# Kernel optimization log

Hardware: AMD Instinct MI355X
Metric: run time of the kernel (lower is better)

The kernel has to match this reference:

```python
import jax, jax.numpy as jnp
import numpy as np

B, N, E, D, H, L = 1024, 64, 1024, 128, 4, 2
C = D // H          # per-head out_channels
K = 5               # options per attribute
LN_EPS = 1e-5


def setup_inputs() -> dict:
    key = jax.random.key(0)
    ks = jax.random.split(key, 22)
    s = 0.05
    inp = {
        'x': jax.random.randint(ks[0], (B, N), 0, K),
        'edge_index': jax.random.randint(ks[1], (2, E), 0, N),
        'edge_attr': jax.random.uniform(ks[2], (E, 1), jnp.float32),
        # tokenizer params
        'attr_emb': jax.random.normal(ks[3], (N, D), jnp.float32) * s,
        'opt_emb': jax.random.normal(ks[4], (N, K, D), jnp.float32) * s,
        'prior': jnp.ones((N, 1), jnp.float32),
        # GATv2 params, stacked over layers
        'Wl': jax.random.normal(ks[5], (L, D, D), jnp.float32) * s,
        'bl': jnp.zeros((L, D), jnp.float32),
        'Wr': jax.random.normal(ks[6], (L, D, D), jnp.float32) * s,
        'br': jnp.zeros((L, D), jnp.float32),
        'We': jax.random.normal(ks[7], (L, 1, D), jnp.float32) * s,
        'att': jax.random.normal(ks[8], (L, H, C), jnp.float32) * s,
        'conv_bias': jnp.zeros((L, D), jnp.float32),
        'ln_g': jnp.ones((L, D), jnp.float32),
        'ln_b': jnp.zeros((L, D), jnp.float32),
        # reliability head
        'W1': jax.random.normal(ks[9], (2 * D, D), jnp.float32) * s,
        'b1': jnp.zeros((D,), jnp.float32),
        'W2': jax.random.normal(ks[10], (D, 1), jnp.float32) * s,
        'b2': jnp.zeros((1,), jnp.float32),
    }
    return inp


def _forward(x, edge_index, edge_attr, attr_emb, opt_emb, prior,
             Wl, bl, Wr, br, We, att, conv_bias, ln_g, ln_b, W1, b1, W2, b2):
    Bb, n = x.shape
    # Tokenizer: token_i = p_i * (E_attr[i] + E_val[i](x_i))
    val = opt_emb[jnp.arange(n)[None, :], x]                 # [B,n,D]
    T0 = (attr_emb[None] + val) * prior[None]                # [B,n,D]

    src, dst = edge_index[0], edge_index[1]
    h = T0
    for l in range(Wl.shape[0]):
        xl = (h @ Wl[l] + bl[l]).reshape(Bb, n, H, C)        # source transform
        xr = (h @ Wr[l] + br[l]).reshape(Bb, n, H, C)        # target transform
        e = (edge_attr @ We[l]).reshape(1, E, H, C)          # edge embedding
        msg = xl[:, src]                                     # [B,E,H,C]
        z = jax.nn.leaky_relu(msg + xr[:, dst] + e, 0.2)
        alpha = jnp.einsum('behc,hc->beh', z, att[l])        # [B,E,H]
        # segment softmax over incoming edges per target node
        mx = jnp.full((Bb, n, H), -jnp.inf, alpha.dtype).at[:, dst].max(alpha)
        ex = jnp.exp(alpha - mx[:, dst])
        den = jnp.zeros((Bb, n, H), alpha.dtype).at[:, dst].add(ex)
        a = ex / den[:, dst]                                 # normalized attention
        out = jnp.zeros((Bb, n, H, C), h.dtype).at[:, dst].add(msg * a[..., None])
        g = out.reshape(Bb, n, D) + conv_bias[l]
        mu = g.mean(-1, keepdims=True)
        var = g.var(-1, keepdims=True)
        g = (g - mu) / jnp.sqrt(var + LN_EPS) * ln_g[l] + ln_b[l]
        g = jax.nn.elu(g)
        h = h + g                                            # residual

    hat_T = jnp.concatenate([T0, h], axis=-1)                # [B,n,2D]
    rel = jax.nn.sigmoid(jax.nn.relu(hat_T @ W1 + b1) @ W2 + b2)[..., 0]  # [B,n]
    rw = rel[..., None]
    f_scale = (h * rw).sum(1) / (rw.sum(1) + 1e-8)           # [B,D]
    return f_scale, rel, hat_T


def reference(x, edge_index, edge_attr, attr_emb, opt_emb, prior,
              Wl, bl, Wr, br, We, att, conv_bias, ln_g, ln_b, W1, b1, W2, b2):
    return _forward(x, edge_index, edge_attr, attr_emb, opt_emb, prior,
                    Wl, bl, Wr, br, We, att, conv_bias, ln_g, ln_b, W1, b1, W2, b2)
```

## Files before the change

### kernel.cpp

```cpp
#include <hip/hip_runtime.h>
#include <hip/hip_bf16.h>

#define Bv 1024
#define Nv 64
#define Ev 1024
#define Dv 128
#define Hv 4
#define Lv 2
#define Kv 5
#define PAD 130

typedef __hip_bfloat16 bf16;
typedef __attribute__((ext_vector_type(8))) short bf16x8_t;
typedef __attribute__((ext_vector_type(4))) float f32x4_t;
typedef __attribute__((ext_vector_type(2))) float f32x2_t;

__device__ __forceinline__ float b2f(bf16 v) { return __bfloat162float(v); }
__device__ __forceinline__ bf16  f2b(float v) { return __float2bfloat16(v); }

__device__ bf16 g_pWl[(size_t)Lv * 2 * Dv * Dv];
__device__ bf16 g_pWr[(size_t)Lv * 2 * Dv * Dv];
__device__ bf16 g_pW1[(size_t)2 * 2 * Dv * Dv];
__device__ float g_K[Lv * Hv];
__device__ unsigned short g_spk[Ev];
__device__ float          g_sea[Ev];
__device__ int            g_off[Nv + 1];

__device__ __forceinline__ f32x2_t unpack2v(unsigned int u) {
    union { unsigned int u; float f; } a, b;
    a.u = u << 16;
    b.u = u & 0xffff0000u;
    return (f32x2_t){a.f, b.f};
}

__device__ __forceinline__ unsigned int pack2v(f32x2_t v) {
    union { bf16 b; unsigned short u; } lo, hi;
    lo.b = f2b(v.x); hi.b = f2b(v.y);
    return (unsigned int)lo.u | ((unsigned int)hi.u << 16);
}

__device__ __forceinline__ bf16x8_t load_a_frag(const bf16* buf, int elem_idx) {
    const unsigned int* p = (const unsigned int*)buf;
    union { bf16x8_t v; unsigned int u[4]; } r;
    int d = elem_idx >> 1;
    r.u[0] = p[d]; r.u[1] = p[d + 1]; r.u[2] = p[d + 2]; r.u[3] = p[d + 3];
    return r.v;
}

__device__ void pack_mat(const float* __restrict__ W, bf16* __restrict__ out,
                         int K, int tid, int nth)
{
    const int total = K * 128;
    for (int e = tid; e < total; e += nth) {
        int f    = e >> 9;
        int rem  = e & 511;
        int lane = rem >> 3;
        int i    = rem & 7;
        int kk   = f >> 3;
        int nt   = f & 7;
        int col  = nt * 16 + (lane & 15);
        int k    = kk * 32 + (lane >> 4) * 8 + i;
        float w  = W[k * 128 + col];
        bf16 hi  = f2b(w);
        out[e]         = hi;
        out[total + e] = f2b(w - b2f(hi));
    }
}

__global__ void prep(const int* __restrict__ edge_index, const float* __restrict__ edge_attr,
                     const float* __restrict__ Wl, const float* __restrict__ Wr,
                     const float* __restrict__ W1, const float* __restrict__ We,
                     const float* __restrict__ att)
{
    const int bid = blockIdx.x;
    if (bid == 0) {
        __shared__ int cnt[Nv];
        int tid = threadIdx.x;
        if (tid < Nv) cnt[tid] = 0;
        __syncthreads();
        for (int e = tid; e < Ev; e += blockDim.x)
            atomicAdd(&cnt[edge_index[Ev + e]], 1);
        __syncthreads();
        if (tid == 0) {
            int s = 0;
            for (int t = 0; t < Nv; ++t) { int c = cnt[t]; g_off[t] = s; cnt[t] = s; s += c; }
            g_off[Nv] = s;
        }
        __syncthreads();
        for (int e = tid; e < Ev; e += blockDim.x) {
            int s = edge_index[e];
            int d = edge_index[Ev + e];
            int pos = atomicAdd(&cnt[d], 1);
            g_spk[pos] = (unsigned short)(s | (d << 6));
            g_sea[pos] = edge_attr[e];
        }
        return;
    }
    const int nth = (gridDim.x - 1) * 256;
    const int tid = (bid - 1) * 256 + threadIdx.x;
    for (int l = 0; l < Lv; ++l) {
        pack_mat(Wl + (size_t)l * Dv * Dv, g_pWl + (size_t)l * 2 * Dv * Dv, Dv, tid, nth);
        pack_mat(Wr + (size_t)l * Dv * Dv, g_pWr + (size_t)l * 2 * Dv * Dv, Dv, tid, nth);
    }
    pack_mat(W1, g_pW1, 2 * Dv, tid, nth);
    if (bid == 1 && threadIdx.x < Lv * Hv) {
        int l = threadIdx.x / Hv, h = threadIdx.x % Hv;
        float k = 0.f;
        for (int c = 0; c < 32; ++c)
            k += att[l * Dv + h * 32 + c] * We[l * Dv + h * 32 + c];
        g_K[threadIdx.x] = 0.2f * k;
    }
}

__global__ __launch_bounds__(512, 2)
void gat_fused(const int* __restrict__ x,
               const float* __restrict__ attr_emb,
               const float* __restrict__ opt_emb, const float* __restrict__ prior,
               const float* __restrict__ bl, const float* __restrict__ br,
               const float* __restrict__ conv_bias, const float* __restrict__ ln_g,
               const float* __restrict__ ln_b,
               const float* __restrict__ b1, const float* __restrict__ W2,
               const float* __restrict__ b2,
               const float* __restrict__ We, const float* __restrict__ att,
               float* __restrict__ out_fscale, float* __restrict__ out_rel,
               float* __restrict__ out_hatT)
{
    const int b = blockIdx.x;
    const int tid = threadIdx.x;

    __shared__ __align__(16) bf16 hs [Nv * PAD];
    __shared__ __align__(16) bf16 xls[Nv * PAD];
    __shared__ __align__(16) bf16 xrs[Nv * PAD];
    __shared__ bf16 alphas[Ev * Hv];
    __shared__ __align__(16) float red [Nv * 8];
    __shared__ __align__(16) float red2[Nv * 8];
    __shared__ __align__(16) float wecol[Dv];
    __shared__ __align__(16) float attv [Dv];
    __shared__ float relbuf[Nv];
    __shared__ __align__(16) unsigned short spk[Ev];
    __shared__ __align__(16) float sea[Ev];
    __shared__ int off[Nv + 1];

    for (int i = tid; i < Ev; i += 512) {
        spk[i] = g_spk[i];
        sea[i] = g_sea[i];
    }
    if (tid < Nv + 1) off[tid] = g_off[tid];
    for (int idx = tid; idx < Nv * Dv; idx += 512) {
        int n = idx >> 7, d = idx & 127;
        float t0 = (attr_emb[n * Dv + d] + opt_emb[(n * Kv + x[b * Nv + n]) * Dv + d])
                   * prior[n];
        hs[n * PAD + d] = f2b(t0);
    }

    for (int l = 0; l < Lv; ++l) {
        if (tid < Dv) {
            wecol[tid] = We[l * Dv + tid];
            attv[tid]  = att[l * Dv + tid];
        }
        __syncthreads();

        {
            const int w = tid >> 6, lane = tid & 63;
            const int row16 = lane & 15, kg = lane >> 4;
            const bf16* pB = (w < 4) ? (g_pWl + (size_t)l * 2 * Dv * Dv)
                                     : (g_pWr + (size_t)l * 2 * Dv * Dv);
            const int wc = (w & 3) * 32;
            bf16* dst = (w < 4) ? xls : xrs;
            const float* bias = (w < 4) ? (bl + l * Dv) : (br + l * Dv);

            #pragma unroll
            for (int nt = 0; nt < 2; ++nt) {
                f32x4_t acc[4];
                #pragma unroll
                for (int mt = 0; mt < 4; ++mt)
                    acc[mt] = (f32x4_t){0.f, 0.f, 0.f, 0.f};

                #pragma unroll
                for (int kk = 0; kk < 4; ++kk) {
                    const int kb = kk * 32 + kg * 8;
                    const int f = kk * 8 + (w & 3) * 2 + nt;
                    bf16x8_t bh  = *(const bf16x8_t*)&pB[(size_t)(f * 64 + lane) * 8];
                    bf16x8_t blo = *(const bf16x8_t*)&pB[Dv * Dv + (size_t)(f * 64 + lane) * 8];
                    #pragma unroll
                    for (int mt = 0; mt < 4; ++mt) {
                        bf16x8_t a = load_a_frag(hs, (mt * 16 + row16) * PAD + kb);
                        acc[mt] = __builtin_amdgcn_mfma_f32_16x16x32_bf16(a, bh,  acc[mt], 0, 0, 0);
                        acc[mt] = __builtin_amdgcn_mfma_f32_16x16x32_bf16(a, blo, acc[mt], 0, 0, 0);
                    }
                }
                const int col = wc + nt * 16 + row16;
                const float bv = bias[col];
                #pragma unroll
                for (int mt = 0; mt < 4; ++mt) {
                    #pragma unroll
                    for (int r = 0; r < 4; ++r) {
                        const int row = mt * 16 + kg * 4 + r;
                        dst[row * PAD + col] = f2b(acc[mt][r] + bv);
                    }
                }
            }
        }
        __syncthreads();

        {
            const int t = tid & 63, h = (tid >> 6) & 3, half = tid >> 8;
            const int ch0 = h * 32 + half * 16;
            f32x2_t dl2 = {0.f, 0.f}, dr2 = {0.f, 0.f};
            #pragma unroll
            for (int c = 0; c < 16; c += 2) {
                f32x2_t a2 = *(const f32x2_t*)&attv[ch0 + c];
                dl2 += a2 * unpack2v(*(const unsigned int*)&xls[t * PAD + ch0 + c]);
                dr2 += a2 * unpack2v(*(const unsigned int*)&xrs[t * PAD + ch0 + c]);
            }
            red [t * 8 + h * 2 + half] = dl2.x + dl2.y;
            red2[t * 8 + h * 2 + half] = dr2.x + dr2.y;
        }
        __syncthreads();

        {
            const int h = (tid >> 6) & 3, half = tid >> 8, lane = tid & 63;
            const float k02 = g_K[l * Hv + h];
            const f32x2_t zero2 = {0.f, 0.f};
            for (int it = 0; it < 8; ++it) {
                int pos = (half * 8 + it) * 64 + lane;
                int pk = spk[pos];
                int s = pk & 63, t = (pk >> 6) & 63;
                float ea = sea[pos];
                f32x2_t ea2 = {ea, ea};
                f32x2_t acc2 = {0.f, 0.f};
                int bs = s * PAD + h * 32, bt = t * PAD + h * 32;
                #pragma unroll
                for (int c = 0; c < 32; c += 2) {
                    f32x2_t xl2 = unpack2v(*(const unsigned int*)&xls[bs + c]);
                    f32x2_t xr2 = unpack2v(*(const unsigned int*)&xrs[bt + c]);
                    f32x2_t we2 = *(const f32x2_t*)&wecol[h * 32 + c];
                    f32x2_t at2 = *(const f32x2_t*)&attv [h * 32 + c];
                    f32x2_t v   = xl2 + xr2 + ea2 * we2;
                    acc2 += at2 * __builtin_elementwise_max(v, zero2);
                }
                float dL = red [s * 8 + h * 2] + red [s * 8 + h * 2 + 1];
                float dR = red2[t * 8 + h * 2] + red2[t * 8 + h * 2 + 1];
                float alpha = 0.2f * (dL + dR) + k02 * ea + 0.8f * (acc2.x + acc2.y);
                alphas[pos * Hv + h] = f2b(alpha);
            }
        }
        __syncthreads();

        {
            const int t = tid & 63, h = (tid >> 6) & 3, half = tid >> 8;
            const int ch0 = h * 32 + half * 16;
            int beg = off[t], end = off[t + 1];
            float mx = -3e38f;
            for (int idx = beg; idx < end; ++idx)
                mx = fmaxf(mx, b2f(alphas[idx * Hv + h]));
            f32x2_t acc2[8];
            #pragma unroll
            for (int j = 0; j < 8; ++j) acc2[j] = (f32x2_t){0.f, 0.f};
            float den = 0.f;
            for (int idx = beg; idx < end; ++idx) {
                int s = spk[idx] & 63;
                float ex = expf(b2f(alphas[idx * Hv + h]) - mx);
                den += ex;
                f32x2_t ex2 = {ex, ex};
                int bs = s * PAD + ch0;
                #pragma unroll
                for (int j = 0; j < 8; ++j)
                    acc2[j] += ex2 * unpack2v(*(const unsigned int*)&xls[bs + 2 * j]);
            }
            float inv_den = (end > beg) ? 1.f / den : 0.f;
            f32x2_t id2 = {inv_den, inv_den};
            f32x2_t sum2 = {0.f, 0.f}, sq2 = {0.f, 0.f};
            #pragma unroll
            for (int j = 0; j < 8; ++j) {
                f32x2_t cb = *(const f32x2_t*)&conv_bias[l * Dv + ch0 + 2 * j];
                f32x2_t g  = acc2[j] * id2 + cb;
                acc2[j] = g;
                sum2 += g; sq2 += g * g;
            }
            red [t * 8 + h * 2 + half] = sum2.x + sum2.y;
            red2[t * 8 + h * 2 + half] = sq2.x + sq2.y;
            __syncthreads();
            float mu = 0.f, ms = 0.f;
            #pragma unroll
            for (int j = 0; j < 8; ++j) { mu += red[t * 8 + j]; ms += red2[t * 8 + j]; }
            mu *= (1.f / 128.f); ms *= (1.f / 128.f);
            float rstd = rsqrtf(ms - mu * mu + 1e-5f);
            f32x2_t mu2 = {mu, mu}, rs2 = {rstd, rstd};
            #pragma unroll
            for (int j = 0; j < 8; ++j) {
                f32x2_t lg = *(const f32x2_t*)&ln_g[l * Dv + ch0 + 2 * j];
                f32x2_t lb = *(const f32x2_t*)&ln_b[l * Dv + ch0 + 2 * j];
                f32x2_t g  = (acc2[j] - mu2) * rs2 * lg + lb;
                g.x = g.x > 0.f ? g.x : (expf(g.x) - 1.f);
                g.y = g.y > 0.f ? g.y : (expf(g.y) - 1.f);
                unsigned int* hp = (unsigned int*)&hs[t * PAD + ch0 + 2 * j];
                f32x2_t hv = unpack2v(*hp) + g;
                *hp = pack2v(hv);
            }
        }
        __syncthreads();
    }

    if (tid < Dv) wecol[tid] = W2[tid];
    for (int idx = tid; idx < Nv * Dv; idx += 512) {
        int n = idx >> 7, d = idx & 127;
        float t0 = (attr_emb[n * Dv + d] + opt_emb[(n * Kv + x[b * Nv + n]) * Dv + d])
                   * prior[n];
        xrs[n * PAD + d] = f2b(t0);
        size_t rb = ((size_t)(b * Nv + n)) * (2 * Dv);
        out_hatT[rb + d]      = t0;
        out_hatT[rb + Dv + d] = b2f(hs[n * PAD + d]);
    }
    __syncthreads();

    {
        const int w = tid >> 6, lane = tid & 63;
        const int row16 = lane & 15, kg = lane >> 4;
        f32x4_t acc[4];
        #pragma unroll
        for (int mt = 0; mt < 4; ++mt)
            acc[mt] = (f32x4_t){0.f, 0.f, 0.f, 0.f};

        #pragma unroll
        for (int kk = 0; kk < 8; ++kk) {
            const bf16* asrc = (kk < 4) ? xrs : hs;
            const int kb = (kk & 3) * 32 + kg * 8;
            const int f = kk * 8 + w;
            bf16x8_t bh  = *(const bf16x8_t*)&g_pW1[(size_t)(f * 64 + lane) * 8];
            bf16x8_t blo = *(const bf16x8_t*)&g_pW1[(size_t)2 * Dv * Dv + (size_t)(f * 64 + lane) * 8];
            #pragma unroll
            for (int mt = 0; mt < 4; ++mt) {
                bf16x8_t a = load_a_frag(asrc, (mt * 16 + row16) * PAD + kb);
                acc[mt] = __builtin_amdgcn_mfma_f32_16x16x32_bf16(a, bh,  acc[mt], 0, 0, 0);
                acc[mt] = __builtin_amdgcn_mfma_f32_16x16x32_bf16(a, blo, acc[mt], 0, 0, 0);
            }
        }
        #pragma unroll
        for (int mt = 0; mt < 4; ++mt) {
            const int col = w * 16 + row16;
            #pragma unroll
            for (int r = 0; r < 4; ++r) {
                const int row = mt * 16 + kg * 4 + r;
                float v = acc[mt][r] + b1[col];
                xls[row * PAD + col] = f2b(v > 0.f ? v : 0.f);
            }
        }
    }
    __syncthreads();

    {
        const int t = tid & 63, h = (tid >> 6) & 3, half = tid >> 8;
        const int ch0 = h * 32 + half * 16;
        f32x2_t s2 = {0.f, 0.f};
        #pragma unroll
        for (int c = 0; c < 16; c += 2) {
            f32x2_t h2 = unpack2v(*(const unsigned int*)&xls[t * PAD + ch0 + c]);
            s2 += h2 * *(const f32x2_t*)&wecol[ch0 + c];
        }
        red[t * 8 + h * 2 + half] = s2.x + s2.y;
        __syncthreads();
        if (h == 0 && half == 0) {
            float z = b2[0];
            #pragma unroll
            for (int j = 0; j < 8; ++j) z += red[t * 8 + j];
            float r = 1.f / (1.f + expf(-z));
            relbuf[t] = r;
            out_rel[b * Nv + t] = r;
        }
    }
    __syncthreads();

    if (tid < Dv) {
        float num = 0.f, den = 0.f;
        for (int n = 0; n < Nv; ++n) {
            float r = relbuf[n];
            num += b2f(hs[n * PAD + tid]) * r;
            den += r;
        }
        out_fscale[b * Dv + tid] = num / (den + 1e-8f);
    }
}

extern "C" void kernel_launch(void* const* d_in, const int* in_sizes, int n_in,
                              void* d_out, int out_size, void* d_ws, size_t ws_size,
                              hipStream_t stream)
{
    const int*   x          = (const int*)  d_in[0];
    const int*   edge_index = (const int*)  d_in[1];
    const float* edge_attr  = (const float*)d_in[2];
    const float* attr_emb   = (const float*)d_in[3];
    const float* opt_emb    = (const float*)d_in[4];
    const float* prior      = (const float*)d_in[5];
    const float* Wl         = (const float*)d_in[6];
    const float* bl         = (const float*)d_in[7];
    const float* Wr         = (const float*)d_in[8];
    const float* br         = (const float*)d_in[9];
    const float* We         = (const float*)d_in[10];
    const float* att        = (const float*)d_in[11];
    const float* conv_bias  = (const float*)d_in[12];
    const float* ln_g       = (const float*)d_in[13];
    const float* ln_b       = (const float*)d_in[14];
    const float* W1         = (const float*)d_in[15];
    const float* b1         = (const float*)d_in[16];
    const float* W2         = (const float*)d_in[17];
    const float* b2         = (const float*)d_in[18];

    float* out        = (float*)d_out;
    float* out_fscale = out;
    float* out_rel    = out + (size_t)Bv * Dv;
    float* out_hatT   = out + (size_t)Bv * Dv + (size_t)Bv * Nv;

    prep<<<129, 256, 0, stream>>>(edge_index, edge_attr, Wl, Wr, W1, We, att);
    gat_fused<<<Bv, 512, 0, stream>>>(x, attr_emb, opt_emb,
                                      prior, bl, br, conv_bias,
                                      ln_g, ln_b, b1, W2, b2, We, att,
                                      out_fscale, out_rel, out_hatT);
}
```

Baseline: 292.2 us.

## Drop target-dependent attention term and read packed edge table from global

Removes the per-target dot product (dR) from the attention logit, since a term constant across a destination node's incoming edges cancels in the softmax. Edge source, target and attribute are packed into one 32-bit word, with the attribute rounded to bf16, and read directly from global memory (L1/L2-cached) instead of being staged into shared memory. Each thread's CSR begin and end offsets are loaded once into registers. This saves shared-memory footprint and some LDS work. The risks are extra global-load latency inside the edge loops and lost precision on the edge attribute.

Measured after the change: 293.3 us. Within noise of the previous version (+0.4%).

```diff
diff --git a/kernel.cpp b/kernel.cpp
--- a/kernel.cpp
+++ b/kernel.cpp
@@ -22,9 +22,8 @@
 __device__ bf16 g_pWr[(size_t)Lv * 2 * Dv * Dv];
 __device__ bf16 g_pW1[(size_t)2 * 2 * Dv * Dv];
 __device__ float g_K[Lv * Hv];
-__device__ unsigned short g_spk[Ev];
-__device__ float          g_sea[Ev];
-__device__ int            g_off[Nv + 1];
+__device__ unsigned int g_etab[Ev];
+__device__ int          g_off[Nv + 1];
 
 __device__ __forceinline__ f32x2_t unpack2v(unsigned int u) {
     union { unsigned int u; float f; } a, b;
@@ -91,8 +90,9 @@
             int s = edge_index[e];
             int d = edge_index[Ev + e];
             int pos = atomicAdd(&cnt[d], 1);
-            g_spk[pos] = (unsigned short)(s | (d << 6));
-            g_sea[pos] = edge_attr[e];
+            union { bf16 b; unsigned short u; } cv;
+            cv.b = f2b(edge_attr[e]);
+            g_etab[pos] = (unsigned int)(s | (d << 6)) | ((unsigned int)cv.u << 16);
         }
         return;
     }
@@ -137,15 +137,11 @@
     __shared__ __align__(16) float wecol[Dv];
     __shared__ __align__(16) float attv [Dv];
     __shared__ float relbuf[Nv];
-    __shared__ __align__(16) unsigned short spk[Ev];
-    __shared__ __align__(16) float sea[Ev];
-    __shared__ int off[Nv + 1];
-
-    for (int i = tid; i < Ev; i += 512) {
-        spk[i] = g_spk[i];
-        sea[i] = g_sea[i];
-    }
-    if (tid < Nv + 1) off[tid] = g_off[tid];
+
+    const int my_t  = tid & 63;
+    const int beg   = g_off[my_t];
+    const int end   = g_off[my_t + 1];
+
     for (int idx = tid; idx < Nv * Dv; idx += 512) {
         int n = idx >> 7, d = idx & 127;
         float t0 = (attr_emb[n * Dv + d] + opt_emb[(n * Kv + x[b * Nv + n]) * Dv + d])
@@ -206,15 +202,13 @@
         {
             const int t = tid & 63, h = (tid >> 6) & 3, half = tid >> 8;
             const int ch0 = h * 32 + half * 16;
-            f32x2_t dl2 = {0.f, 0.f}, dr2 = {0.f, 0.f};
+            f32x2_t dl2 = {0.f, 0.f};
             #pragma unroll
             for (int c = 0; c < 16; c += 2) {
                 f32x2_t a2 = *(const f32x2_t*)&attv[ch0 + c];
                 dl2 += a2 * unpack2v(*(const unsigned int*)&xls[t * PAD + ch0 + c]);
-                dr2 += a2 * unpack2v(*(const unsigned int*)&xrs[t * PAD + ch0 + c]);
-            }
-            red [t * 8 + h * 2 + half] = dl2.x + dl2.y;
-            red2[t * 8 + h * 2 + half] = dr2.x + dr2.y;
+            }
+            red[t * 8 + h * 2 + half] = dl2.x + dl2.y;
         }
         __syncthreads();
 
@@ -224,9 +218,10 @@
             const f32x2_t zero2 = {0.f, 0.f};
             for (int it = 0; it < 8; ++it) {
                 int pos = (half * 8 + it) * 64 + lane;
-                int pk = spk[pos];
-                int s = pk & 63, t = (pk >> 6) & 63;
-                float ea = sea[pos];
+                unsigned int et = g_etab[pos];
+                int s = et & 63, t = (et >> 6) & 63;
+                union { unsigned int u; float f; } ec; ec.u = et & 0xffff0000u;
+                float ea = ec.f;
                 f32x2_t ea2 = {ea, ea};
                 f32x2_t acc2 = {0.f, 0.f};
                 int bs = s * PAD + h * 32, bt = t * PAD + h * 32;
@@ -239,18 +234,16 @@
                     f32x2_t v   = xl2 + xr2 + ea2 * we2;
                     acc2 += at2 * __builtin_elementwise_max(v, zero2);
                 }
-                float dL = red [s * 8 + h * 2] + red [s * 8 + h * 2 + 1];
-                float dR = red2[t * 8 + h * 2] + red2[t * 8 + h * 2 + 1];
-                float alpha = 0.2f * (dL + dR) + k02 * ea + 0.8f * (acc2.x + acc2.y);
+                float dL = red[s * 8 + h * 2] + red[s * 8 + h * 2 + 1];
+                float alpha = 0.2f * dL + k02 * ea + 0.8f * (acc2.x + acc2.y);
                 alphas[pos * Hv + h] = f2b(alpha);
             }
         }
         __syncthreads();
 
         {
-            const int t = tid & 63, h = (tid >> 6) & 3, half = tid >> 8;
+            const int t = my_t, h = (tid >> 6) & 3, half = tid >> 8;
             const int ch0 = h * 32 + half * 16;
-            int beg = off[t], end = off[t + 1];
             float mx = -3e38f;
             for (int idx = beg; idx < end; ++idx)
                 mx = fmaxf(mx, b2f(alphas[idx * Hv + h]));
@@ -259,7 +252,7 @@
             for (int j = 0; j < 8; ++j) acc2[j] = (f32x2_t){0.f, 0.f};
             float den = 0.f;
             for (int idx = beg; idx < end; ++idx) {
-                int s = spk[idx] & 63;
+                int s = (int)(g_etab[idx] & 63u);
                 float ex = expf(b2f(alphas[idx * Hv + h]) - mx);
                 den += ex;
                 f32x2_t ex2 = {ex, ex};
```
